# Performance work log

Measured on AMD Instinct MI355X. Metric: run time of the kernel, lower is better.

Reference implementation:

```python
import jax, jax.numpy as jnp
import numpy as np

B, L, N, D, C, WS, NH = 32, 64, 1024, 512, 8192, 3, 16
HD = D // NH          # head_dim = 32
HID = 2 * D           # MLP expansion = 2


def _ln(x, g, b, eps=1e-5):
    m = jnp.mean(x, -1, keepdims=True)
    v = jnp.mean((x - m) ** 2, -1, keepdims=True)
    return (x - m) * jax.lax.rsqrt(v + eps) * g + b


def setup_inputs() -> dict:
    key = jax.random.key(0)
    ks = jax.random.split(key, 16)
    r = lambda i, shape, s=0.02: jax.random.normal(ks[i], shape, jnp.float32) * s
    return dict(
        visual_features=jax.random.normal(ks[0], (B, N, D), jnp.float32),
        targets=jax.random.randint(ks[1], (B, L), 0, C),
        pad_id=1,
        char_embed=r(2, (C, D), 1.0),
        ln1_g=jnp.ones(D), ln1_b=jnp.zeros(D),
        in_proj_w=r(3, (3 * D, D)), in_proj_b=jnp.zeros(3 * D),
        out_w=r(4, (D, D)), out_b=jnp.zeros(D),
        fc1_w=r(5, (HID, D)), fc1_b=jnp.zeros(HID),
        fc2_w=r(6, (D, HID)), fc2_b=jnp.zeros(D),
        ln2_g=jnp.ones(D), ln2_b=jnp.zeros(D),
        left_token=r(7, (1, 1, D)), right_token=r(8, (1, 1, D)),
        q_w=r(9, (D, D)), q_b=jnp.zeros(D),
        kv_w=r(10, (2 * D, D)), kv_b=jnp.zeros(2 * D),
        proj_w=r(11, (D, D)), proj_b=jnp.zeros(D),
        lnq_g=jnp.ones(D), lnq_b=jnp.zeros(D),
        lnkv_g=jnp.ones(D), lnkv_b=jnp.zeros(D),
        head_w=r(12, (C, D)), head_b=jnp.zeros(C),
    )


def reference(visual_features, targets, pad_id, char_embed, ln1_g, ln1_b,
              in_proj_w, in_proj_b, out_w, out_b, fc1_w, fc1_b, fc2_w, fc2_b,
              ln2_g, ln2_b, left_token, right_token, q_w, q_b, kv_w, kv_b,
              proj_w, proj_b, lnq_g, lnq_b, lnkv_g, lnkv_b, head_w, head_b):
    # --- build left/right context windows via gather (vectorizes the python loop) ---
    padded = jnp.pad(targets, ((0, 0), (WS, WS)), constant_values=pad_id)
    li = jnp.arange(L)[:, None] + jnp.arange(WS)[None, :]      # (L, WS)
    left_ids = padded[:, li]                                   # (B, L, WS)
    right_ids = padded[:, li + WS + 1]                         # (B, L, WS)

    def encode(ids, tok):
        x = char_embed[ids] + tok                 # (B, L, WS, D)
        x = x.reshape(B * L, WS, D)               # (M, WS, D)
        xn = _ln(x, ln1_g, ln1_b)
        qkv = xn @ in_proj_w.T + in_proj_b
        q, k, v = jnp.split(qkv, 3, -1)
        sh = lambda t: t.reshape(B * L, WS, NH, HD).transpose(0, 2, 1, 3)
        q, k, v = sh(q), sh(k), sh(v)
        a = jax.nn.softmax(jnp.einsum('mhqd,mhkd->mhqk', q, k) * HD ** -0.5, -1)
        o = jnp.einsum('mhqk,mhkd->mhqd', a, v).transpose(0, 2, 1, 3).reshape(B * L, WS, D)
        x = x + o @ out_w.T + out_b
        h = jax.nn.gelu(_ln(x, ln2_g, ln2_b) @ fc1_w.T + fc1_b, approximate=False)
        x = x + h @ fc2_w.T + fc2_b
        return x.mean(1).reshape(B, L, D)

    def cross(qs):
        q = _ln(qs, lnq_g, lnq_b) @ q_w.T + q_b
        kv = _ln(visual_features, lnkv_g, lnkv_b) @ kv_w.T + kv_b
        k, v = jnp.split(kv, 2, -1)
        q = q.reshape(B, L, NH, HD).transpose(0, 2, 1, 3)
        k = k.reshape(B, N, NH, HD).transpose(0, 2, 1, 3)
        v = v.reshape(B, N, NH, HD).transpose(0, 2, 1, 3)
        a = jax.nn.softmax(jnp.einsum('bhld,bhnd->bhln', q, k) * HD ** -0.5, -1)
        o = jnp.einsum('bhln,bhnd->bhld', a, v).transpose(0, 2, 1, 3).reshape(B, L, D)
        return o @ proj_w.T + proj_b

    left_enc = encode(left_ids, left_token)
    right_enc = encode(right_ids, right_token)
    left_feat = left_enc + cross(left_enc)
    right_feat = right_enc + cross(right_enc)
    sgm_left = left_feat @ head_w.T + head_b      # (B, L, C)
    sgm_right = right_feat @ head_w.T + head_b    # (B, L, C)
    return sgm_left, sgm_right, targets
```

## Files before the change

kernel.cpp:

```cpp
#include <hip/hip_runtime.h>
#include <hip/hip_bf16.h>
#include <cstdint>
#include <cstddef>


typedef __attribute__((ext_vector_type(8))) short s16x8;
typedef __attribute__((ext_vector_type(8))) unsigned short u16x8;
typedef __attribute__((ext_vector_type(4))) unsigned short u16x4;
typedef __attribute__((ext_vector_type(4))) float f32x4;

__device__ __forceinline__ float b2f(unsigned short u) {
  union { unsigned int i; float f; } c; c.i = ((unsigned int)u) << 16; return c.f;
}
__device__ __forceinline__ unsigned short f2b(float f) {
  union { float f; unsigned int i; } c; c.f = f;
  unsigned int x = c.i;
  return (unsigned short)((x + 0x7FFFu + ((x >> 16) & 1u)) >> 16);
}

#define GLOAD16(gp, lp)                                                        \
  __builtin_amdgcn_global_load_lds(                                           \
      (const __attribute__((address_space(1))) void*)(gp),                    \
      (__attribute__((address_space(3))) void*)(lp), 16, 0, 0)

__global__ void cvt_all(const float* __restrict__ s0, const float* __restrict__ s1,
                        const float* __restrict__ s2, const float* __restrict__ s3,
                        const float* __restrict__ s4, const float* __restrict__ s5,
                        const float* __restrict__ s6, const float* __restrict__ s7,
                        unsigned short* __restrict__ d) {
  int c = blockIdx.x * 256 + threadIdx.x;
  if (c >= 1835008) return;
  int e = c * 4;
  const float* sp; int off;
  if      (e <  786432) { sp = s0; off = 0; }
  else if (e < 1048576) { sp = s1; off =  786432; }
  else if (e < 1572864) { sp = s2; off = 1048576; }
  else if (e < 2097152) { sp = s3; off = 1572864; }
  else if (e < 2359296) { sp = s4; off = 2097152; }
  else if (e < 2883584) { sp = s5; off = 2359296; }
  else if (e < 3145728) { sp = s6; off = 2883584; }
  else                  { sp = s7; off = 3145728; }
  float4 v = *(const float4*)(sp + (e - off));
  u16x4 o; o[0] = f2b(v.x); o[1] = f2b(v.y); o[2] = f2b(v.z); o[3] = f2b(v.w);
  *(u16x4*)(d + e) = o;
}

__global__ void embed_k(const int* __restrict__ targets, const int* __restrict__ pad_p,
                        const float* __restrict__ ce, const float* __restrict__ ltok,
                        const float* __restrict__ rtok, unsigned short* __restrict__ x) {
  int idx = blockIdx.x * 256 + threadIdx.x;
  if (idx >= 12288 * 128) return;
  int row = idx >> 7, d4 = idx & 127;
  int side = row >= 6144;
  int rem = row - side * 6144;
  int pos = rem / 3, w = rem - pos * 3;
  int b = pos >> 6, l = pos & 63;
  int id;
  if (!side) { int ti = l + w - 3; id = (ti >= 0) ? targets[(b << 6) + ti] : *pad_p; }
  else       { int ti = l + w + 1; id = (ti < 64) ? targets[(b << 6) + ti] : *pad_p; }
  float4 cv = ((const float4*)ce)[(size_t)id * 128 + d4];
  float4 tv = ((const float4*)(side ? rtok : ltok))[d4];
  u16x4 o; o[0] = f2b(cv.x + tv.x); o[1] = f2b(cv.y + tv.y);
  o[2] = f2b(cv.z + tv.z); o[3] = f2b(cv.w + tv.w);
  *(u16x4*)(x + (size_t)idx * 4) = o;
}

template<int INBF>
__global__ __launch_bounds__(256) void ln_rows(const void* __restrict__ in,
    const float* __restrict__ g, const float* __restrict__ b,
    unsigned short* __restrict__ out, int M) {
  int row = blockIdx.x * 4 + (threadIdx.x >> 6);
  int lane = threadIdx.x & 63;
  float vv[8];
  if (INBF) {
    u16x8 v8 = *(const u16x8*)((const unsigned short*)in + (size_t)row * 512 + lane * 8);
#pragma unroll
    for (int j = 0; j < 8; ++j) vv[j] = b2f(v8[j]);
  } else {
    const float* rp = (const float*)in + (size_t)row * 512;
    float4 v0 = ((const float4*)rp)[lane * 2];
    float4 v1 = ((const float4*)rp)[lane * 2 + 1];
    vv[0] = v0.x; vv[1] = v0.y; vv[2] = v0.z; vv[3] = v0.w;
    vv[4] = v1.x; vv[5] = v1.y; vv[6] = v1.z; vv[7] = v1.w;
  }
  float s = 0.f, ss = 0.f;
#pragma unroll
  for (int j = 0; j < 8; ++j) { s += vv[j]; ss += vv[j] * vv[j]; }
#pragma unroll
  for (int o = 1; o < 64; o <<= 1) { s += __shfl_xor(s, o); ss += __shfl_xor(ss, o); }
  float mean = s * (1.0f / 512.0f);
  float var = ss * (1.0f / 512.0f) - mean * mean;
  float inv = rsqrtf(var + 1e-5f);
  int c = lane * 8;
  u16x8 o8;
#pragma unroll
  for (int j = 0; j < 8; ++j) o8[j] = f2b((vv[j] - mean) * inv * g[c + j] + b[c + j]);
  *(u16x8*)(out + (size_t)row * 512 + c) = o8;
}

template<int RES, int GELU, int OUTBF, int KVT>
__global__ __launch_bounds__(256) void gemm128(
    const unsigned short* __restrict__ A, const unsigned short* __restrict__ Bt,
    const float* __restrict__ bias, const void* __restrict__ res,
    void* __restrict__ outp, int M, int N, int K) {
  __shared__ unsigned short sA[2][8192];
  __shared__ unsigned short sB[2][8192];
  const int tid = threadIdx.x;
  const int nbx = gridDim.x;
  int id = blockIdx.y * nbx + blockIdx.x;
  {
    const int nwg = nbx * gridDim.y;
    if ((nwg & 7) == 0) id = (id & 7) * (nwg >> 3) + (id >> 3);
  }
  const int bm = (id / nbx) * 128, bn = (id % nbx) * 128;
  const int wave = tid >> 6, lane = tid & 63;
  const int wr = (wave >> 1) * 64, wc = (wave & 1) * 64;
  const int lrow = lane & 15, g = lane >> 4;
  f32x4 acc[4][4] = {};
  const int xoff = (((((lrow & 1) << 2) | g) ^ ((lrow >> 1) & 7)) << 3);
  const int baseA = ((wr >> 1) + (lrow >> 1)) * 64 + xoff;
  const int baseB = ((wc >> 1) + (lrow >> 1)) * 64 + xoff;
  const int slot8 = (tid & 7) ^ ((tid >> 3) & 7);
  const int srow = ((tid >> 3) << 1) + (slot8 >> 2);
  const int scol = (slot8 & 3) << 3;
  const unsigned short* gA = A + (size_t)(bm + srow) * K + scol;
  const unsigned short* gB = Bt + (size_t)(bn + srow) * K + scol;
  const int NT = K >> 6;

#define STAGE128(buf, kt)                                                      \
  { _Pragma("unroll")                                                          \
    for (int h = 0; h < 2; ++h) {                                              \
      _Pragma("unroll")                                                        \
      for (int i = 0; i < 2; ++i) {                                            \
        GLOAD16(gA + (size_t)(i * 64) * K + (kt) * 64 + h * 32,                \
                &sA[buf][h * 4096 + i * 2048 + wave * 512]);                   \
        GLOAD16(gB + (size_t)(i * 64) * K + (kt) * 64 + h * 32,                \
                &sB[buf][h * 4096 + i * 2048 + wave * 512]);                   \
      }                                                                        \
    } }

  STAGE128(0, 0);
  __syncthreads();
  int cur = 0;
  for (int kt = 0; kt < NT; ++kt) {
    s16x8 a0[4], b0[4];
#pragma unroll
    for (int m = 0; m < 4; ++m) a0[m] = *(const s16x8*)&sA[cur][baseA + m * 512];
#pragma unroll
    for (int n = 0; n < 4; ++n) b0[n] = *(const s16x8*)&sB[cur][baseB + n * 512];
    if (kt + 1 < NT) STAGE128(cur ^ 1, kt + 1);
    __builtin_amdgcn_s_setprio(1);
#pragma unroll
    for (int m = 0; m < 4; ++m)
#pragma unroll
      for (int n = 0; n < 4; ++n)
        acc[m][n] = __builtin_amdgcn_mfma_f32_16x16x32_bf16(b0[n], a0[m], acc[m][n], 0, 0, 0);
    __builtin_amdgcn_s_setprio(0);
    s16x8 a1[4], b1[4];
#pragma unroll
    for (int m = 0; m < 4; ++m) a1[m] = *(const s16x8*)&sA[cur][4096 + baseA + m * 512];
#pragma unroll
    for (int n = 0; n < 4; ++n) b1[n] = *(const s16x8*)&sB[cur][4096 + baseB + n * 512];
    __builtin_amdgcn_s_setprio(1);
#pragma unroll
    for (int m = 0; m < 4; ++m)
#pragma unroll
      for (int n = 0; n < 4; ++n)
        acc[m][n] = __builtin_amdgcn_mfma_f32_16x16x32_bf16(b1[n], a1[m], acc[m][n], 0, 0, 0);
    __builtin_amdgcn_s_setprio(0);
    __syncthreads();
    cur ^= 1;
  }
#undef STAGE128

  const int orow_ = bm + wr + lrow;
  const int ocol_ = bn + wc + g * 4;
#pragma unroll
  for (int m = 0; m < 4; ++m) {
    const int row = orow_ + m * 16;
#pragma unroll
    for (int n = 0; n < 4; ++n) {
      const int col = ocol_ + n * 16;
      f32x4 v = acc[m][n];
      f32x4 b4 = *(const f32x4*)(bias + col);
      v += b4;
      if (GELU) {
#pragma unroll
        for (int r = 0; r < 4; ++r)
          v[r] = 0.5f * v[r] * (1.0f + erff(v[r] * 0.70710678118654752f));
      }
      if (RES == 1) v += *(const f32x4*)((const float*)res + (size_t)row * N + col);
      if (RES == 2) {
        u16x4 r4 = *(const u16x4*)((const unsigned short*)res + (size_t)row * N + col);
#pragma unroll
        for (int r = 0; r < 4; ++r) v[r] += b2f(r4[r]);
      }
      if (KVT) {
        int bb = row >> 10, nn = row & 1023;
        unsigned short* Kp = (unsigned short*)outp;
        unsigned short* VpT = Kp + 16777216u;
        if (col < 512) {
          int hh = col >> 5, dd = col & 31;
          u16x4 o4;
#pragma unroll
          for (int r = 0; r < 4; ++r) o4[r] = f2b(v[r]);
          *(u16x4*)(Kp + (((size_t)(bb * 16 + hh)) * 1024 + nn) * 32 + dd) = o4;
        } else {
          int cc = col - 512, hh = cc >> 5, dd = cc & 31;
#pragma unroll
          for (int r = 0; r < 4; ++r)
            VpT[(((size_t)(bb * 16 + hh)) * 32 + dd + r) * 1024 + nn] = f2b(v[r]);
        }
      } else if (OUTBF) {
        u16x4 o4;
#pragma unroll
        for (int r = 0; r < 4; ++r) o4[r] = f2b(v[r]);
        *(u16x4*)((unsigned short*)outp + (size_t)row * N + col) = o4;
      } else {
        *(f32x4*)((float*)outp + (size_t)row * N + col) = v;
      }
    }
  }
}

__global__ __launch_bounds__(256) void winattn(const unsigned short* __restrict__ qkv,
                                               unsigned short* __restrict__ o) {
  int g = blockIdx.x * 256 + threadIdx.x;
  if (g >= 4096 * 48) return;
  int i = g % 3;
  int t = g / 3;
  int h = t & 15;
  int sp = t >> 4;
  const unsigned short* base = qkv + (size_t)sp * 4608 + h * 32;
  float qv[32];
  {
    const u16x8* qp = (const u16x8*)(base + (size_t)i * 1536);
#pragma unroll
    for (int c = 0; c < 4; ++c) {
      u16x8 v = qp[c];
#pragma unroll
      for (int j = 0; j < 8; ++j) qv[c * 8 + j] = b2f(v[j]);
    }
  }
  float s[3];
#pragma unroll
  for (int j3 = 0; j3 < 3; ++j3) {
    const u16x8* kp = (const u16x8*)(base + (size_t)j3 * 1536 + 512);
    float acc = 0.f;
#pragma unroll
    for (int c = 0; c < 4; ++c) {
      u16x8 v = kp[c];
#pragma unroll
      for (int j = 0; j < 8; ++j) acc += qv[c * 8 + j] * b2f(v[j]);
    }
    s[j3] = acc * 0.17677669529663687f;
  }
  float mx = fmaxf(s[0], fmaxf(s[1], s[2]));
  float e0 = __expf(s[0] - mx), e1 = __expf(s[1] - mx), e2 = __expf(s[2] - mx);
  float inv = 1.0f / (e0 + e1 + e2);
  float a0 = e0 * inv, a1 = e1 * inv, a2 = e2 * inv;
  unsigned short* op = o + (size_t)(sp * 3 + i) * 512 + h * 32;
  const u16x8* v0p = (const u16x8*)(base + 1024);
  const u16x8* v1p = (const u16x8*)(base + 1536 + 1024);
  const u16x8* v2p = (const u16x8*)(base + 3072 + 1024);
#pragma unroll
  for (int c = 0; c < 4; ++c) {
    u16x8 x0 = v0p[c], x1 = v1p[c], x2 = v2p[c];
    u16x8 ov;
#pragma unroll
    for (int j = 0; j < 8; ++j)
      ov[j] = f2b(a0 * b2f(x0[j]) + a1 * b2f(x1[j]) + a2 * b2f(x2[j]));
    *(u16x8*)(op + c * 8) = ov;
  }
}

__global__ void mean3(const unsigned short* __restrict__ x, float* __restrict__ enc) {
  int i = blockIdx.x * 256 + threadIdx.x;
  if (i >= 4096 * 128) return;
  int p = i >> 7, d4 = i & 127;
  u16x4 a = *(const u16x4*)(x + ((size_t)(p * 3 + 0) * 512 + d4 * 4));
  u16x4 b = *(const u16x4*)(x + ((size_t)(p * 3 + 1) * 512 + d4 * 4));
  u16x4 c = *(const u16x4*)(x + ((size_t)(p * 3 + 2) * 512 + d4 * 4));
  float4 o;
  o.x = (b2f(a[0]) + b2f(b[0]) + b2f(c[0])) * (1.0f / 3.0f);
  o.y = (b2f(a[1]) + b2f(b[1]) + b2f(c[1])) * (1.0f / 3.0f);
  o.z = (b2f(a[2]) + b2f(b[2]) + b2f(c[2])) * (1.0f / 3.0f);
  o.w = (b2f(a[3]) + b2f(b[3]) + b2f(c[3])) * (1.0f / 3.0f);
  ((float4*)enc)[i] = o;
}

__global__ __launch_bounds__(512) void crossattn_mfma(const unsigned short* __restrict__ q,
    const unsigned short* __restrict__ Kp, const unsigned short* __restrict__ VpT,
    unsigned short* __restrict__ o) {
  __shared__ unsigned short Plds[8][2][16 * 40];
  const int bh = blockIdx.x;
  const int b = bh >> 4, h = bh & 15;
  const int tid = threadIdx.x;
  const int w = tid >> 6, lane = tid & 63;
  const int side = w >> 2, wsub = w & 3;
  const int ql = lane & 15, g = lane >> 4;
  const int qrow = side * 2048 + b * 64 + wsub * 16 + ql;
  const float SC = 0.17677669529663687f;
  s16x8 qf;
  {
    u16x8 qv8 = *(const u16x8*)(q + (size_t)qrow * 512 + h * 32 + g * 8);
#pragma unroll
    for (int j = 0; j < 8; ++j) qf[j] = (short)f2b(b2f(qv8[j]) * SC);
  }
  const unsigned short* kbase = Kp + ((size_t)(b * 16 + h) * 1024) * 32;
  const unsigned short* vbase = VpT + ((size_t)(b * 16 + h) * 32) * 1024;
  f32x4 oacc0 = {}, oacc1 = {};
  float m_run = -1e30f, l_part = 0.f;
  for (int kv0 = 0; kv0 < 1024; kv0 += 32) {
    const int pp = (kv0 >> 5) & 1;
    s16x8 kf0 = *(const s16x8*)(kbase + (size_t)(kv0 + ql) * 32 + g * 8);
    s16x8 kf1 = *(const s16x8*)(kbase + (size_t)(kv0 + 16 + ql) * 32 + g * 8);
    f32x4 z = {0.f, 0.f, 0.f, 0.f};
    f32x4 s0 = __builtin_amdgcn_mfma_f32_16x16x32_bf16(kf0, qf, z, 0, 0, 0);
    f32x4 s1 = __builtin_amdgcn_mfma_f32_16x16x32_bf16(kf1, qf, z, 0, 0, 0);
    float cm = fmaxf(fmaxf(fmaxf(s0[0], s0[1]), fmaxf(s0[2], s0[3])),
                     fmaxf(fmaxf(s1[0], s1[1]), fmaxf(s1[2], s1[3])));
    cm = fmaxf(cm, __shfl_xor(cm, 16));
    cm = fmaxf(cm, __shfl_xor(cm, 32));
    float m_new = fmaxf(m_run, cm);
    float corr = __expf(m_run - m_new);
    m_run = m_new;
    float p0[4], p1[4], ps = 0.f;
#pragma unroll
    for (int r = 0; r < 4; ++r) {
      p0[r] = __expf(s0[r] - m_new);
      p1[r] = __expf(s1[r] - m_new);
      ps += p0[r] + p1[r];
    }
    l_part = l_part * corr + ps;
    oacc0 *= corr; oacc1 *= corr;
    u16x4 w0, w1;
#pragma unroll
    for (int r = 0; r < 4; ++r) { w0[r] = f2b(p0[r]); w1[r] = f2b(p1[r]); }
    *(u16x4*)&Plds[w][pp][ql * 40 + g * 4] = w0;
    *(u16x4*)&Plds[w][pp][ql * 40 + 16 + g * 4] = w1;
    __syncthreads();
    s16x8 pf = *(const s16x8*)&Plds[w][pp][ql * 40 + g * 8];
    s16x8 vf0 = *(const s16x8*)(vbase + (size_t)ql * 1024 + kv0 + g * 8);
    s16x8 vf1 = *(const s16x8*)(vbase + (size_t)(16 + ql) * 1024 + kv0 + g * 8);
    oacc0 = __builtin_amdgcn_mfma_f32_16x16x32_bf16(vf0, pf, oacc0, 0, 0, 0);
    oacc1 = __builtin_amdgcn_mfma_f32_16x16x32_bf16(vf1, pf, oacc1, 0, 0, 0);
  }
  float lf = l_part;
  lf += __shfl_xor(lf, 16);
  lf += __shfl_xor(lf, 32);
  float inv = 1.0f / lf;
  unsigned short* op = o + (size_t)qrow * 512 + h * 32;
  u16x4 ov0, ov1;
#pragma unroll
  for (int r = 0; r < 4; ++r) {
    ov0[r] = f2b(oacc0[r] * inv);
    ov1[r] = f2b(oacc1[r] * inv);
  }
  *(u16x4*)(op + g * 4) = ov0;
  *(u16x4*)(op + 16 + g * 4) = ov1;
}

__global__ void tail_targets(const int* __restrict__ t, float* __restrict__ out) {
  int i = blockIdx.x * 256 + threadIdx.x;
  if (i < 2048) out[33554432 + i] = (float)t[i];
}

extern "C" void kernel_launch(void* const* d_in, const int* in_sizes, int n_in,
                              void* d_out, int out_size, void* d_ws, size_t ws_size,
                              hipStream_t stream) {
  const float* visual   = (const float*)d_in[0];
  const int*   targets  = (const int*)d_in[1];
  const int*   pad_p    = (const int*)d_in[2];
  const float* char_emb = (const float*)d_in[3];
  const float* ln1_g = (const float*)d_in[4];
  const float* ln1_b = (const float*)d_in[5];
  const float* in_proj_w = (const float*)d_in[6];
  const float* in_proj_b = (const float*)d_in[7];
  const float* out_w = (const float*)d_in[8];
  const float* out_b = (const float*)d_in[9];
  const float* fc1_w = (const float*)d_in[10];
  const float* fc1_b = (const float*)d_in[11];
  const float* fc2_w = (const float*)d_in[12];
  const float* fc2_b = (const float*)d_in[13];
  const float* ln2_g = (const float*)d_in[14];
  const float* ln2_b = (const float*)d_in[15];
  const float* ltok  = (const float*)d_in[16];
  const float* rtok  = (const float*)d_in[17];
  const float* q_w   = (const float*)d_in[18];
  const float* q_b   = (const float*)d_in[19];
  const float* kv_w  = (const float*)d_in[20];
  const float* kv_b  = (const float*)d_in[21];
  const float* proj_w = (const float*)d_in[22];
  const float* proj_b = (const float*)d_in[23];
  const float* lnq_g = (const float*)d_in[24];
  const float* lnq_b = (const float*)d_in[25];
  const float* lnkv_g = (const float*)d_in[26];
  const float* lnkv_b = (const float*)d_in[27];
  const float* head_w = (const float*)d_in[28];
  const float* head_b = (const float*)d_in[29];

  char* ws = (char*)d_ws;
  unsigned short* W    = (unsigned short*)ws;
  unsigned short* XB   = (unsigned short*)(ws + 14680064ull);
  unsigned short* KP   = (unsigned short*)(ws + 14680064ull);
  unsigned short* A1   = (unsigned short*)(ws + 39845888ull);
  unsigned short* B1   = (unsigned short*)(ws + 52428800ull);
  unsigned short* QKV  = (unsigned short*)(ws + 77594624ull);
  float*          ENC  = (float*)(ws + 115343360ull);
  unsigned short* VIS  = (unsigned short*)(ws + 123731968ull);
  unsigned short* Q    = (unsigned short*)(ws + 157286400ull);
  unsigned short* OC   = (unsigned short*)(ws + 165675008ull);
  unsigned short* FEAT = (unsigned short*)(ws + 169869312ull);
  unsigned short* LNQ  = (unsigned short*)(ws + 174063616ull);
  unsigned short* VPT  = KP + 16777216u;

  unsigned short* Wip   = W;
  unsigned short* Wfc1  = W + 1048576;
  unsigned short* Wfc2  = W + 1572864;
  unsigned short* Wq    = W + 2097152;
  unsigned short* Wkv   = W + 2359296;
  unsigned short* Wproj = W + 2883584;
  unsigned short* Whead = W + 3145728;
  unsigned short* Wout  = W + 786432;

  cvt_all<<<dim3(7168), dim3(256), 0, stream>>>(in_proj_w, out_w, fc1_w, fc2_w,
                                                q_w, kv_w, proj_w, head_w, W);

  embed_k<<<dim3(6144), dim3(256), 0, stream>>>(targets, pad_p, char_emb, ltok, rtok, XB);
  ln_rows<1><<<dim3(3072), dim3(256), 0, stream>>>(XB, ln1_g, ln1_b, A1, 12288);
  gemm128<0,0,1,0><<<dim3(12, 96), dim3(256), 0, stream>>>(A1, Wip, in_proj_b, nullptr, QKV, 12288, 1536, 512);
  winattn<<<dim3(768), dim3(256), 0, stream>>>(QKV, B1);
  gemm128<2,0,1,0><<<dim3(4, 96), dim3(256), 0, stream>>>(B1, Wout, out_b, XB, XB, 12288, 512, 512);
  ln_rows<1><<<dim3(3072), dim3(256), 0, stream>>>(XB, ln2_g, ln2_b, A1, 12288);
  gemm128<0,1,1,0><<<dim3(8, 96), dim3(256), 0, stream>>>(A1, Wfc1, fc1_b, nullptr, B1, 12288, 1024, 512);
  gemm128<2,0,1,0><<<dim3(4, 96), dim3(256), 0, stream>>>(B1, Wfc2, fc2_b, XB, XB, 12288, 512, 1024);
  mean3<<<dim3(2048), dim3(256), 0, stream>>>(XB, ENC);

  ln_rows<0><<<dim3(8192), dim3(256), 0, stream>>>(visual, lnkv_g, lnkv_b, VIS, 32768);
  gemm128<0,0,1,1><<<dim3(8, 256), dim3(256), 0, stream>>>(VIS, Wkv, kv_b, nullptr, KP, 32768, 1024, 512);
  ln_rows<0><<<dim3(1024), dim3(256), 0, stream>>>(ENC, lnq_g, lnq_b, LNQ, 4096);
  gemm128<0,0,1,0><<<dim3(4, 32), dim3(256), 0, stream>>>(LNQ, Wq, q_b, nullptr, Q, 4096, 512, 512);
  crossattn_mfma<<<dim3(512), dim3(512), 0, stream>>>(Q, KP, VPT, OC);
  gemm128<1,0,1,0><<<dim3(4, 32), dim3(256), 0, stream>>>(OC, Wproj, proj_b, ENC, FEAT, 4096, 512, 512);

  gemm128<0,0,0,0><<<dim3(64, 32), dim3(256), 0, stream>>>(FEAT, Whead, head_b, nullptr, (float*)d_out, 4096, 8192, 512);
  tail_targets<<<dim3(8), dim3(256), 0, stream>>>(targets, (float*)d_out);
}
```

Baseline: 390.3 us.

## Switch GEMM to three-stage BK=32 LDS pipeline with one barrier per step

Changes the gemm128 main loop from a double-buffered BK=64 scheme to a triple-buffered BK=32 ring. It prefetches two tiles ahead with global_load_lds, waits with explicit vmcnt counts, and uses one s_barrier per iteration instead of a trailing __syncthreads. The goal is more overlap of global loads with MFMA work and less stall at each barrier. In exchange, each barrier covers half as much MFMA work, and LDS use drops from 64KB to 48KB, which may allow more resident blocks.

```diff
diff --git a/kernel.cpp b/kernel.cpp
--- a/kernel.cpp
+++ b/kernel.cpp
@@ -103,8 +103,8 @@
     const unsigned short* __restrict__ A, const unsigned short* __restrict__ Bt,
     const float* __restrict__ bias, const void* __restrict__ res,
     void* __restrict__ outp, int M, int N, int K) {
-  __shared__ unsigned short sA[2][8192];
-  __shared__ unsigned short sB[2][8192];
+  __shared__ unsigned short sA[3][4096];
+  __shared__ unsigned short sB[3][4096];
   const int tid = threadIdx.x;
   const int nbx = gridDim.x;
   int id = blockIdx.y * nbx + blockIdx.x;
@@ -125,53 +125,43 @@
   const int scol = (slot8 & 3) << 3;
   const unsigned short* gA = A + (size_t)(bm + srow) * K + scol;
   const unsigned short* gB = Bt + (size_t)(bn + srow) * K + scol;
-  const int NT = K >> 6;
-
-#define STAGE128(buf, kt)                                                      \
+  const int NT = K >> 5;
+
+#define STG(slot, kt)                                                          \
   { _Pragma("unroll")                                                          \
-    for (int h = 0; h < 2; ++h) {                                              \
-      _Pragma("unroll")                                                        \
-      for (int i = 0; i < 2; ++i) {                                            \
-        GLOAD16(gA + (size_t)(i * 64) * K + (kt) * 64 + h * 32,                \
-                &sA[buf][h * 4096 + i * 2048 + wave * 512]);                   \
-        GLOAD16(gB + (size_t)(i * 64) * K + (kt) * 64 + h * 32,                \
-                &sB[buf][h * 4096 + i * 2048 + wave * 512]);                   \
-      }                                                                        \
+    for (int i = 0; i < 2; ++i) {                                              \
+      GLOAD16(gA + (size_t)(i * 64) * K + (kt) * 32, &sA[slot][i * 2048 + wave * 512]); \
+      GLOAD16(gB + (size_t)(i * 64) * K + (kt) * 32, &sB[slot][i * 2048 + wave * 512]); \
     } }
 
-  STAGE128(0, 0);
-  __syncthreads();
-  int cur = 0;
-  for (int kt = 0; kt < NT; ++kt) {
-    s16x8 a0[4], b0[4];
-#pragma unroll
-    for (int m = 0; m < 4; ++m) a0[m] = *(const s16x8*)&sA[cur][baseA + m * 512];
-#pragma unroll
-    for (int n = 0; n < 4; ++n) b0[n] = *(const s16x8*)&sB[cur][baseB + n * 512];
-    if (kt + 1 < NT) STAGE128(cur ^ 1, kt + 1);
+  STG(0, 0);
+  STG(1, 1);
+  int sl = 0;
+  for (int t = 0; t < NT; ++t) {
+    if (t < NT - 1) asm volatile("s_waitcnt vmcnt(4)" ::: "memory");
+    else            asm volatile("s_waitcnt vmcnt(0)" ::: "memory");
+    __builtin_amdgcn_s_barrier();
+    __builtin_amdgcn_sched_barrier(0);
+    if (t + 2 < NT) {
+      int sl2 = sl - 1; if (sl2 < 0) sl2 = 2;
+      STG(sl2, t + 2);
+    }
+    s16x8 av[4], bv[4];
+#pragma unroll
+    for (int m = 0; m < 4; ++m) av[m] = *(const s16x8*)&sA[sl][baseA + m * 512];
+#pragma unroll
+    for (int n = 0; n < 4; ++n) bv[n] = *(const s16x8*)&sB[sl][baseB + n * 512];
     __builtin_amdgcn_s_setprio(1);
 #pragma unroll
     for (int m = 0; m < 4; ++m)
 #pragma unroll
       for (int n = 0; n < 4; ++n)
-        acc[m][n] = __builtin_amdgcn_mfma_f32_16x16x32_bf16(b0[n], a0[m], acc[m][n], 0, 0, 0);
+        acc[m][n] = __builtin_amdgcn_mfma_f32_16x16x32_bf16(bv[n], av[m], acc[m][n], 0, 0, 0);
     __builtin_amdgcn_s_setprio(0);
-    s16x8 a1[4], b1[4];
-#pragma unroll
-    for (int m = 0; m < 4; ++m) a1[m] = *(const s16x8*)&sA[cur][4096 + baseA + m * 512];
-#pragma unroll
-    for (int n = 0; n < 4; ++n) b1[n] = *(const s16x8*)&sB[cur][4096 + baseB + n * 512];
-    __builtin_amdgcn_s_setprio(1);
-#pragma unroll
-    for (int m = 0; m < 4; ++m)
-#pragma unroll
-      for (int n = 0; n < 4; ++n)
-        acc[m][n] = __builtin_amdgcn_mfma_f32_16x16x32_bf16(b1[n], a1[m], acc[m][n], 0, 0, 0);
-    __builtin_amdgcn_s_setprio(0);
-    __syncthreads();
-    cur ^= 1;
-  }
-#undef STAGE128
+    asm volatile("s_waitcnt lgkmcnt(0)" ::: "memory");
+    sl = (sl == 2) ? 0 : sl + 1;
+  }
+#undef STG
 
   const int orow_ = bm + wr + lrow;
   const int ocol_ = bn + wc + g * 4;
@@ -416,13 +406,13 @@
   unsigned short* VPT  = KP + 16777216u;
 
   unsigned short* Wip   = W;
+  unsigned short* Wout  = W + 786432;
   unsigned short* Wfc1  = W + 1048576;
   unsigned short* Wfc2  = W + 1572864;
   unsigned short* Wq    = W + 2097152;
   unsigned short* Wkv   = W + 2359296;
   unsigned short* Wproj = W + 2883584;
   unsigned short* Whead = W + 3145728;
-  unsigned short* Wout  = W + 786432;
 
   cvt_all<<<dim3(7168), dim3(256), 0, stream>>>(in_proj_w, out_w, fc1_w, fc2_w,
                                                 q_w, kv_w, proj_w, head_w, W);
```

Result: no change. 393.9 us (+0.9%).
